# Kernel optimization log

Hardware: AMD Instinct MI355X
Metric: run time of the kernel (lower is better)

## Reference

```python
import jax, jax.numpy as jnp
import numpy as np

B = 8192
N_IN = 16 * 12 * 64  # 12288
H0, H1, H2 = 256, 32, 32
OUTPUT_SCALE = 300.0
WDL_SCALE = 200.0


def setup_inputs() -> dict:
    key = jax.random.key(0)
    ks = jax.random.split(key, 12)
    # In real NNUE these are ~30-hot binary vectors; math is identical for dense rand.
    white_features = (jax.random.uniform(ks[0], (B, N_IN)) < 0.0025).astype(jnp.float32)
    black_features = (jax.random.uniform(ks[1], (B, N_IN)) < 0.0025).astype(jnp.float32)
    side = jax.random.randint(ks[2], (B,), 0, 2).astype(bool)
    ft_std = np.sqrt(2.0 / (22 + H1))
    ft_w = jax.random.normal(ks[3], (H0, N_IN)) * ft_std
    ft_b = jnp.zeros((H0,))
    def xavier(k, fan_out, fan_in):
        std = np.sqrt(2.0 / (fan_in + fan_out))
        return jax.random.normal(k, (fan_out, fan_in)) * std
    l1_w = xavier(ks[4], H1, 2 * H0)
    l1_b = jnp.zeros((H1,))
    l2_w = xavier(ks[5], H2, H1)
    l2_b = jnp.zeros((H2,))
    l3_w = xavier(ks[6], 1, H2)
    l3_b = jnp.zeros((1,))
    return {"white_features": white_features, "black_features": black_features,
            "side": side, "ft_w": ft_w, "ft_b": ft_b, "l1_w": l1_w, "l1_b": l1_b,
            "l2_w": l2_w, "l2_b": l2_b, "l3_w": l3_w, "l3_b": l3_b}


def reference(white_features, black_features, side, ft_w, ft_b,
              l1_w, l1_b, l2_w, l2_b, l3_w, l3_b):
    w = white_features @ ft_w.T + ft_b  # [B, H0]
    b = black_features @ ft_w.T + ft_b  # [B, H0]
    s = side[:, None]  # [B, 1] bool
    # side-to-move first: white -> [w, b], black -> [b, w]
    acc = jnp.where(s, jnp.concatenate([w, b], axis=1),
                    jnp.concatenate([b, w], axis=1))  # [B, 2*H0]
    o0 = jnp.clip(acc, 0.0, 1.0)
    o1 = jnp.clip(o0 @ l1_w.T + l1_b, 0.0, 1.0)
    o2 = jnp.clip(o1 @ l2_w.T + l2_b, 0.0, 1.0)
    o3 = (o2 @ l3_w.T + l3_b) * OUTPUT_SCALE  # [B, 1]
    return jax.nn.sigmoid(o3 / WDL_SCALE)
```

## Files before the change

### kernel.cpp

```cpp
#include <hip/hip_runtime.h>
#include <math.h>


#define NIN   12288
#define NF4   3072
#define FPT   12
#define H0    256
#define MAXF  192

__global__ __launch_bounds__(256) void transpose_ftw(const float* __restrict__ src,
                                                     float* __restrict__ dst) {
    __shared__ float tile[32][33];
    const int jb = blockIdx.x * 32;
    const int hb = blockIdx.y * 32;
    const int tx = threadIdx.x;
    const int ty = threadIdx.y;
#pragma unroll
    for (int r = 0; r < 32; r += 8)
        tile[ty + r][tx] = src[(size_t)(hb + ty + r) * NIN + jb + tx];
    __syncthreads();
#pragma unroll
    for (int r = 0; r < 32; r += 8)
        dst[(size_t)(jb + ty + r) * H0 + hb + tx] = tile[tx][ty + r];
}

__global__ __launch_bounds__(256) void zero_counts(int* __restrict__ cnts, int n) {
    const int i = blockIdx.x * 256 + threadIdx.x;
    if (i < n) cnts[i] = 0;
}

__device__ __forceinline__ void scanv(uint4 u, int i,
                                      int* __restrict__ cnts,
                                      int* __restrict__ lists) {
    if (u.x | u.y | u.z | u.w) {
        const int s  = i / NF4;
        const int jb = (i - s * NF4) << 2;
        int* lst = lists + (size_t)s * MAXF;
        int* c   = cnts + s;
        if (u.x) { int p = atomicAdd(c, 1); if (p < MAXF) lst[p] = jb + 0; }
        if (u.y) { int p = atomicAdd(c, 1); if (p < MAXF) lst[p] = jb + 1; }
        if (u.z) { int p = atomicAdd(c, 1); if (p < MAXF) lst[p] = jb + 2; }
        if (u.w) { int p = atomicAdd(c, 1); if (p < MAXF) lst[p] = jb + 3; }
    }
}

__global__ __launch_bounds__(256) void scan_kernel(const uint4* __restrict__ white,
                                                   const uint4* __restrict__ black,
                                                   int* __restrict__ cnts,
                                                   int* __restrict__ lists,
                                                   int total)
{
    const int stride = gridDim.x * 256;
    int i = blockIdx.x * 256 + threadIdx.x;
    int* cnts_b  = cnts;
    const int B = total / NF4;
    for (; i + 3 * stride < total; i += 4 * stride) {
        const uint4 w0 = white[i];
        const uint4 w1 = white[i + stride];
        const uint4 w2 = white[i + 2 * stride];
        const uint4 w3 = white[i + 3 * stride];
        const uint4 b0 = black[i];
        const uint4 b1 = black[i + stride];
        const uint4 b2 = black[i + 2 * stride];
        const uint4 b3 = black[i + 3 * stride];
        scanv(w0, i,              cnts_b, lists);
        scanv(w1, i + stride,     cnts_b, lists);
        scanv(w2, i + 2 * stride, cnts_b, lists);
        scanv(w3, i + 3 * stride, cnts_b, lists);
        scanv(b0, i + B * NF4,              cnts_b, lists);
        scanv(b1, i + stride + B * NF4,     cnts_b, lists);
        scanv(b2, i + 2 * stride + B * NF4, cnts_b, lists);
        scanv(b3, i + 3 * stride + B * NF4, cnts_b, lists);
    }
    for (; i < total; i += stride) {
        scanv(white[i], i, cnts_b, lists);
        scanv(black[i], i + B * NF4, cnts_b, lists);
    }
}

__global__ __launch_bounds__(256) void gather_kernel(
    const int* __restrict__ side,
    const float* __restrict__ ftw,
    const float* __restrict__ ft_b,
    const float* __restrict__ l1_w,
    const float* __restrict__ l1_b,
    const float* __restrict__ l2_w,
    const float* __restrict__ l2_b,
    const float* __restrict__ l3_w,
    const float* __restrict__ l3_b,
    const int* __restrict__ cnts,
    const int* __restrict__ lists,
    float* __restrict__ out,
    int B)
{
    __shared__ int w_list[MAXF];
    __shared__ int b_list[MAXF];
    __shared__ float sh_o0[512] __attribute__((aligned(16)));
    __shared__ float sh_o1[32];
    __shared__ float sh_o2[32];

    const int s   = blockIdx.x;
    const int tid = threadIdx.x;

    const int wn = min(cnts[s], MAXF);
    const int bn = min(cnts[B + s], MAXF);
    if (tid < wn) w_list[tid] = lists[(size_t)s * MAXF + tid];
    if (tid < bn) b_list[tid] = lists[(size_t)(B + s) * MAXF + tid];
    __syncthreads();

    const float bias = ft_b[tid];
    const float* col = ftw + tid;
    float wacc = bias;
    float bacc = bias;
    {
        int k = 0;
        for (; k + 8 <= wn; k += 8) {
            const float f0 = col[(size_t)w_list[k]     * H0];
            const float f1 = col[(size_t)w_list[k + 1] * H0];
            const float f2 = col[(size_t)w_list[k + 2] * H0];
            const float f3 = col[(size_t)w_list[k + 3] * H0];
            const float f4 = col[(size_t)w_list[k + 4] * H0];
            const float f5 = col[(size_t)w_list[k + 5] * H0];
            const float f6 = col[(size_t)w_list[k + 6] * H0];
            const float f7 = col[(size_t)w_list[k + 7] * H0];
            wacc += ((f0 + f1) + (f2 + f3)) + ((f4 + f5) + (f6 + f7));
        }
        for (; k < wn; ++k) wacc += col[(size_t)w_list[k] * H0];
        k = 0;
        for (; k + 8 <= bn; k += 8) {
            const float f0 = col[(size_t)b_list[k]     * H0];
            const float f1 = col[(size_t)b_list[k + 1] * H0];
            const float f2 = col[(size_t)b_list[k + 2] * H0];
            const float f3 = col[(size_t)b_list[k + 3] * H0];
            const float f4 = col[(size_t)b_list[k + 4] * H0];
            const float f5 = col[(size_t)b_list[k + 5] * H0];
            const float f6 = col[(size_t)b_list[k + 6] * H0];
            const float f7 = col[(size_t)b_list[k + 7] * H0];
            bacc += ((f0 + f1) + (f2 + f3)) + ((f4 + f5) + (f6 + f7));
        }
        for (; k < bn; ++k) bacc += col[(size_t)b_list[k] * H0];
    }
    const float ow = fminf(fmaxf(wacc, 0.f), 1.f);
    const float ob = fminf(fmaxf(bacc, 0.f), 1.f);
    const bool sd = (side[s] != 0);
    sh_o0[tid]       = sd ? ow : ob;
    sh_o0[256 + tid] = sd ? ob : ow;
    __syncthreads();

    {
        const int o = tid >> 3;
        const int p = tid & 7;
        const float4* wp = (const float4*)(l1_w + (o * 512 + p * 64));
        const float4* xp = (const float4*)(sh_o0 + p * 64);
        float sum = 0.f;
#pragma unroll
        for (int i = 0; i < 16; ++i) {
            const int v = (2 * p + i) & 15;
            float4 w4 = wp[v];
            float4 x4 = xp[v];
            sum += w4.x * x4.x + w4.y * x4.y + w4.z * x4.z + w4.w * x4.w;
        }
        sum += __shfl_down(sum, 4, 8);
        sum += __shfl_down(sum, 2, 8);
        sum += __shfl_down(sum, 1, 8);
        if (p == 0) sh_o1[o] = fminf(fmaxf(sum + l1_b[o], 0.f), 1.f);
    }
    __syncthreads();

    if (tid < 32) {
        float sum = 0.f;
#pragma unroll
        for (int k = 0; k < 32; ++k) sum += l2_w[tid * 32 + k] * sh_o1[k];
        sh_o2[tid] = fminf(fmaxf(sum + l2_b[tid], 0.f), 1.f);
    }
    __syncthreads();

    if (tid < 32) {
        float p = l3_w[tid] * sh_o2[tid];
        p += __shfl_down(p, 16, 32);
        p += __shfl_down(p, 8, 32);
        p += __shfl_down(p, 4, 32);
        p += __shfl_down(p, 2, 32);
        p += __shfl_down(p, 1, 32);
        if (tid == 0) {
            const float o3  = (p + l3_b[0]) * 300.0f;
            const float sig = 1.0f / (1.0f + expf(-o3 / 200.0f));
            out[s] = sig;
        }
    }
}

template <bool TRANSPOSED>
__global__ __launch_bounds__(256) void nnue_kernel(
    const float* __restrict__ white, const float* __restrict__ black,
    const int* __restrict__ side, const float* __restrict__ ftw,
    const float* __restrict__ ft_b, const float* __restrict__ l1_w,
    const float* __restrict__ l1_b, const float* __restrict__ l2_w,
    const float* __restrict__ l2_b, const float* __restrict__ l3_w,
    const float* __restrict__ l3_b, float* __restrict__ out)
{
    __shared__ int w_list[MAXF];
    __shared__ int b_list[MAXF];
    __shared__ int w_cnt, b_cnt;
    __shared__ float sh_o0[512] __attribute__((aligned(16)));
    __shared__ float sh_o1[32];
    __shared__ float sh_o2[32];
    const int s = blockIdx.x, tid = threadIdx.x;
    if (tid == 0) { w_cnt = 0; b_cnt = 0; }
    __syncthreads();
    const uint4* wrow = (const uint4*)(white + (size_t)s * NIN);
    const uint4* brow = (const uint4*)(black + (size_t)s * NIN);
#pragma unroll
    for (int i = 0; i < FPT; ++i) {
        const int v = i * 256 + tid;
        uint4 u = wrow[v];
        if (u.x | u.y | u.z | u.w) {
            if (u.x) { int p = atomicAdd(&w_cnt, 1); if (p < MAXF) w_list[p] = v * 4 + 0; }
            if (u.y) { int p = atomicAdd(&w_cnt, 1); if (p < MAXF) w_list[p] = v * 4 + 1; }
            if (u.z) { int p = atomicAdd(&w_cnt, 1); if (p < MAXF) w_list[p] = v * 4 + 2; }
            if (u.w) { int p = atomicAdd(&w_cnt, 1); if (p < MAXF) w_list[p] = v * 4 + 3; }
        }
        uint4 b = brow[v];
        if (b.x | b.y | b.z | b.w) {
            if (b.x) { int p = atomicAdd(&b_cnt, 1); if (p < MAXF) b_list[p] = v * 4 + 0; }
            if (b.y) { int p = atomicAdd(&b_cnt, 1); if (p < MAXF) b_list[p] = v * 4 + 1; }
            if (b.z) { int p = atomicAdd(&b_cnt, 1); if (p < MAXF) b_list[p] = v * 4 + 2; }
            if (b.w) { int p = atomicAdd(&b_cnt, 1); if (p < MAXF) b_list[p] = v * 4 + 3; }
        }
    }
    __syncthreads();
    const int wn = min(w_cnt, MAXF), bn = min(b_cnt, MAXF);
    const float bias = ft_b[tid];
    float wacc = bias, bacc = bias;
    for (int k = 0; k < wn; ++k) {
        const int j = w_list[k];
        wacc += TRANSPOSED ? ftw[(size_t)j * H0 + tid] : ftw[(size_t)tid * NIN + j];
    }
    for (int k = 0; k < bn; ++k) {
        const int j = b_list[k];
        bacc += TRANSPOSED ? ftw[(size_t)j * H0 + tid] : ftw[(size_t)tid * NIN + j];
    }
    const float ow = fminf(fmaxf(wacc, 0.f), 1.f);
    const float ob = fminf(fmaxf(bacc, 0.f), 1.f);
    const bool sd = (side[s] != 0);
    sh_o0[tid] = sd ? ow : ob;
    sh_o0[256 + tid] = sd ? ob : ow;
    __syncthreads();
    {
        const int o = tid >> 3, p = tid & 7;
        const float4* wp = (const float4*)(l1_w + (o * 512 + p * 64));
        const float4* xp = (const float4*)(sh_o0 + p * 64);
        float sum = 0.f;
#pragma unroll
        for (int i = 0; i < 16; ++i) {
            const int v = (2 * p + i) & 15;
            float4 w4 = wp[v]; float4 x4 = xp[v];
            sum += w4.x * x4.x + w4.y * x4.y + w4.z * x4.z + w4.w * x4.w;
        }
        sum += __shfl_down(sum, 4, 8);
        sum += __shfl_down(sum, 2, 8);
        sum += __shfl_down(sum, 1, 8);
        if (p == 0) sh_o1[o] = fminf(fmaxf(sum + l1_b[o], 0.f), 1.f);
    }
    __syncthreads();
    if (tid < 32) {
        float sum = 0.f;
#pragma unroll
        for (int k = 0; k < 32; ++k) sum += l2_w[tid * 32 + k] * sh_o1[k];
        sh_o2[tid] = fminf(fmaxf(sum + l2_b[tid], 0.f), 1.f);
    }
    __syncthreads();
    if (tid < 32) {
        float p = l3_w[tid] * sh_o2[tid];
        p += __shfl_down(p, 16, 32);
        p += __shfl_down(p, 8, 32);
        p += __shfl_down(p, 4, 32);
        p += __shfl_down(p, 2, 32);
        p += __shfl_down(p, 1, 32);
        if (tid == 0) {
            const float o3 = (p + l3_b[0]) * 300.0f;
            out[s] = 1.0f / (1.0f + expf(-o3 / 200.0f));
        }
    }
}

extern "C" void kernel_launch(void* const* d_in, const int* in_sizes, int n_in,
                              void* d_out, int out_size, void* d_ws, size_t ws_size,
                              hipStream_t stream) {
    const float* white = (const float*)d_in[0];
    const float* black = (const float*)d_in[1];
    const int*   side  = (const int*)d_in[2];
    const float* ft_w  = (const float*)d_in[3];
    const float* ft_b  = (const float*)d_in[4];
    const float* l1_w  = (const float*)d_in[5];
    const float* l1_b  = (const float*)d_in[6];
    const float* l2_w  = (const float*)d_in[7];
    const float* l2_b  = (const float*)d_in[8];
    const float* l3_w  = (const float*)d_in[9];
    const float* l3_b  = (const float*)d_in[10];
    float*       out   = (float*)d_out;

    const int B = in_sizes[2];
    const size_t t_floats   = (size_t)NIN * H0;
    const size_t cnt_ints   = (size_t)2 * B;
    const size_t list_ints  = (size_t)2 * B * MAXF;
    const size_t need_bytes = t_floats * 4 + (cnt_ints + list_ints) * 4;

    if (ws_size >= need_bytes) {
        float* ftw_t = (float*)d_ws;
        int*   cnts  = (int*)((char*)d_ws + t_floats * 4);
        int*   lists = cnts + cnt_ints;
        const int total = B * NF4;

        hipLaunchKernelGGL(zero_counts, dim3((int)((cnt_ints + 255) / 256)), dim3(256),
                           0, stream, cnts, (int)cnt_ints);
        hipLaunchKernelGGL(transpose_ftw, dim3(NIN / 32, H0 / 32), dim3(32, 8), 0, stream,
                           ft_w, ftw_t);
        hipLaunchKernelGGL(scan_kernel, dim3(2048), dim3(256), 0, stream,
                           (const uint4*)white, (const uint4*)black, cnts, lists, total);
        hipLaunchKernelGGL(gather_kernel, dim3(B), dim3(256), 0, stream,
                           side, ftw_t, ft_b, l1_w, l1_b, l2_w, l2_b, l3_w, l3_b,
                           cnts, lists, out, B);
    } else if (ws_size >= t_floats * 4) {
        float* ftw_t = (float*)d_ws;
        hipLaunchKernelGGL(transpose_ftw, dim3(NIN / 32, H0 / 32), dim3(32, 8), 0, stream,
                           ft_w, ftw_t);
        hipLaunchKernelGGL((nnue_kernel<true>), dim3(B), dim3(256), 0, stream,
                           white, black, side, ftw_t, ft_b, l1_w, l1_b, l2_w, l2_b, l3_w, l3_b, out);
    } else {
        hipLaunchKernelGGL((nnue_kernel<false>), dim3(B), dim3(256), 0, stream,
                           white, black, side, ft_w, ft_b, l1_w, l1_b, l2_w, l2_b, l3_w, l3_b, out);
    }
}
```

Before: 913.6 us.

## Replace global atomic feature lists with per-row nibble bitmasks decoded in gather

The scan kernel now writes one 4-bit mask byte per float4 of input instead of doing global atomics to build per-sample index lists. The gather kernel reads that row's mask bytes and decodes the set bits into shared-memory lists using shared atomics. This removes the zero_counts launch and the global atomic contention. In exchange it writes a dense bitmap (about 2*B*3072 bytes) and adds per-block decode work, and the feature order in the list is now nondeterministic, which can change float summation order.

```diff
diff --git a/kernel.cpp b/kernel.cpp
--- a/kernel.cpp
+++ b/kernel.cpp
@@ -4,6 +4,7 @@
 
 #define NIN   12288
 #define NF4   3072
+#define NDW   768
 #define FPT   12
 #define H0    256
 #define MAXF  192
@@ -24,36 +25,19 @@
         dst[(size_t)(jb + ty + r) * H0 + hb + tx] = tile[tx][ty + r];
 }
 
-__global__ __launch_bounds__(256) void zero_counts(int* __restrict__ cnts, int n) {
-    const int i = blockIdx.x * 256 + threadIdx.x;
-    if (i < n) cnts[i] = 0;
-}
-
-__device__ __forceinline__ void scanv(uint4 u, int i,
-                                      int* __restrict__ cnts,
-                                      int* __restrict__ lists) {
-    if (u.x | u.y | u.z | u.w) {
-        const int s  = i / NF4;
-        const int jb = (i - s * NF4) << 2;
-        int* lst = lists + (size_t)s * MAXF;
-        int* c   = cnts + s;
-        if (u.x) { int p = atomicAdd(c, 1); if (p < MAXF) lst[p] = jb + 0; }
-        if (u.y) { int p = atomicAdd(c, 1); if (p < MAXF) lst[p] = jb + 1; }
-        if (u.z) { int p = atomicAdd(c, 1); if (p < MAXF) lst[p] = jb + 2; }
-        if (u.w) { int p = atomicAdd(c, 1); if (p < MAXF) lst[p] = jb + 3; }
-    }
+__device__ __forceinline__ unsigned char mask4(uint4 u) {
+    return (unsigned char)((u.x ? 1u : 0u) | (u.y ? 2u : 0u) |
+                           (u.z ? 4u : 0u) | (u.w ? 8u : 0u));
 }
 
 __global__ __launch_bounds__(256) void scan_kernel(const uint4* __restrict__ white,
                                                    const uint4* __restrict__ black,
-                                                   int* __restrict__ cnts,
-                                                   int* __restrict__ lists,
+                                                   unsigned char* __restrict__ wbm,
+                                                   unsigned char* __restrict__ bbm,
                                                    int total)
 {
     const int stride = gridDim.x * 256;
     int i = blockIdx.x * 256 + threadIdx.x;
-    int* cnts_b  = cnts;
-    const int B = total / NF4;
     for (; i + 3 * stride < total; i += 4 * stride) {
         const uint4 w0 = white[i];
         const uint4 w1 = white[i + stride];
@@ -63,18 +47,18 @@
         const uint4 b1 = black[i + stride];
         const uint4 b2 = black[i + 2 * stride];
         const uint4 b3 = black[i + 3 * stride];
-        scanv(w0, i,              cnts_b, lists);
-        scanv(w1, i + stride,     cnts_b, lists);
-        scanv(w2, i + 2 * stride, cnts_b, lists);
-        scanv(w3, i + 3 * stride, cnts_b, lists);
-        scanv(b0, i + B * NF4,              cnts_b, lists);
-        scanv(b1, i + stride + B * NF4,     cnts_b, lists);
-        scanv(b2, i + 2 * stride + B * NF4, cnts_b, lists);
-        scanv(b3, i + 3 * stride + B * NF4, cnts_b, lists);
+        wbm[i]              = mask4(w0);
+        wbm[i + stride]     = mask4(w1);
+        wbm[i + 2 * stride] = mask4(w2);
+        wbm[i + 3 * stride] = mask4(w3);
+        bbm[i]              = mask4(b0);
+        bbm[i + stride]     = mask4(b1);
+        bbm[i + 2 * stride] = mask4(b2);
+        bbm[i + 3 * stride] = mask4(b3);
     }
     for (; i < total; i += stride) {
-        scanv(white[i], i, cnts_b, lists);
-        scanv(black[i], i + B * NF4, cnts_b, lists);
+        wbm[i] = mask4(white[i]);
+        bbm[i] = mask4(black[i]);
     }
 }
 
@@ -88,13 +72,13 @@
     const float* __restrict__ l2_b,
     const float* __restrict__ l3_w,
     const float* __restrict__ l3_b,
-    const int* __restrict__ cnts,
-    const int* __restrict__ lists,
-    float* __restrict__ out,
-    int B)
+    const unsigned char* __restrict__ wbm,
+    const unsigned char* __restrict__ bbm,
+    float* __restrict__ out)
 {
     __shared__ int w_list[MAXF];
     __shared__ int b_list[MAXF];
+    __shared__ int w_cnt, b_cnt;
     __shared__ float sh_o0[512] __attribute__((aligned(16)));
     __shared__ float sh_o1[32];
     __shared__ float sh_o2[32];
@@ -102,11 +86,35 @@
     const int s   = blockIdx.x;
     const int tid = threadIdx.x;
 
-    const int wn = min(cnts[s], MAXF);
-    const int bn = min(cnts[B + s], MAXF);
-    if (tid < wn) w_list[tid] = lists[(size_t)s * MAXF + tid];
-    if (tid < bn) b_list[tid] = lists[(size_t)(B + s) * MAXF + tid];
-    __syncthreads();
+    if (tid == 0) { w_cnt = 0; b_cnt = 0; }
+    __syncthreads();
+
+    const unsigned* wrow = (const unsigned*)(wbm + (size_t)s * NF4);
+    const unsigned* brow = (const unsigned*)(bbm + (size_t)s * NF4);
+#pragma unroll
+    for (int q = 0; q < 3; ++q) {
+        const int d = q * 256 + tid;
+        unsigned v = wrow[d];
+        while (v) {
+            const int bpos = __ffs(v) - 1;
+            const int j = ((d * 4 + (bpos >> 3)) << 2) + (bpos & 7);
+            const int p = atomicAdd(&w_cnt, 1);
+            if (p < MAXF) w_list[p] = j;
+            v &= v - 1;
+        }
+        unsigned vb = brow[d];
+        while (vb) {
+            const int bpos = __ffs(vb) - 1;
+            const int j = ((d * 4 + (bpos >> 3)) << 2) + (bpos & 7);
+            const int p = atomicAdd(&b_cnt, 1);
+            if (p < MAXF) b_list[p] = j;
+            vb &= vb - 1;
+        }
+    }
+    __syncthreads();
+
+    const int wn = min(w_cnt, MAXF);
+    const int bn = min(b_cnt, MAXF);
 
     const float bias = ft_b[tid];
     const float* col = ftw + tid;
@@ -184,8 +192,7 @@
         p += __shfl_down(p, 1, 32);
         if (tid == 0) {
             const float o3  = (p + l3_b[0]) * 300.0f;
-            const float sig = 1.0f / (1.0f + expf(-o3 / 200.0f));
-            out[s] = sig;
+            out[s] = 1.0f / (1.0f + expf(-o3 / 200.0f));
         }
     }
 }
@@ -301,27 +308,24 @@
     float*       out   = (float*)d_out;
 
     const int B = in_sizes[2];
-    const size_t t_floats   = (size_t)NIN * H0;
-    const size_t cnt_ints   = (size_t)2 * B;
-    const size_t list_ints  = (size_t)2 * B * MAXF;
-    const size_t need_bytes = t_floats * 4 + (cnt_ints + list_ints) * 4;
-
-    if (ws_size >= need_bytes) {
-        float* ftw_t = (float*)d_ws;
-        int*   cnts  = (int*)((char*)d_ws + t_floats * 4);
-        int*   lists = cnts + cnt_ints;
+    const size_t t_bytes  = (size_t)NIN * H0 * 4;
+    const size_t bm_bytes = (size_t)B * NF4;
+    const size_t need     = t_bytes + 2 * bm_bytes;
+
+    if (ws_size >= need) {
+        float*         ftw_t = (float*)d_ws;
+        unsigned char* wbm   = (unsigned char*)d_ws + t_bytes;
+        unsigned char* bbm   = wbm + bm_bytes;
         const int total = B * NF4;
 
-        hipLaunchKernelGGL(zero_counts, dim3((int)((cnt_ints + 255) / 256)), dim3(256),
-                           0, stream, cnts, (int)cnt_ints);
         hipLaunchKernelGGL(transpose_ftw, dim3(NIN / 32, H0 / 32), dim3(32, 8), 0, stream,
                            ft_w, ftw_t);
         hipLaunchKernelGGL(scan_kernel, dim3(2048), dim3(256), 0, stream,
-                           (const uint4*)white, (const uint4*)black, cnts, lists, total);
+                           (const uint4*)white, (const uint4*)black, wbm, bbm, total);
         hipLaunchKernelGGL(gather_kernel, dim3(B), dim3(256), 0, stream,
                            side, ftw_t, ft_b, l1_w, l1_b, l2_w, l2_b, l3_w, l3_b,
-                           cnts, lists, out, B);
-    } else if (ws_size >= t_floats * 4) {
+                           wbm, bbm, out);
+    } else if (ws_size >= t_bytes) {
         float* ftw_t = (float*)d_ws;
         hipLaunchKernelGGL(transpose_ftw, dim3(NIN / 32, H0 / 32), dim3(32, 8), 0, stream,
                            ft_w, ftw_t);
```

Result: slower. 944.5 us (+3.4%).
